# Kernel tuning notes

Measured on AMD Instinct MI355X. Metric: run time of the kernel, lower is better.

The kernel has to match this reference:

```python
import jax, jax.numpy as jnp
import numpy as np

N = 100000      # nodes
E = 300000      # directed edges (avg degree ~3, ogbn-arxiv-like sparsity)
F_IN = 128      # ogbn-arxiv node features
H = 256         # hidden
C = 40          # ogbn-arxiv classes
L = 6           # num_layers
BN_EPS = 1e-5


def setup_inputs() -> dict:
    key = jax.random.key(0)
    ks = jax.random.split(key, 12)
    x = jax.random.normal(ks[0], (N, F_IN), jnp.float32)
    edge_index = jax.random.randint(ks[1], (2, E), 0, N, dtype=jnp.int32)
    s_in = 1.0 / np.sqrt(F_IN)
    s_h = 1.0 / np.sqrt(H)
    return {
        "x": x,
        "edge_index": edge_index,
        "w_in": jax.random.normal(ks[2], (F_IN, H), jnp.float32) * s_in,
        "b_in": jnp.zeros((H,), jnp.float32),
        "conv_w": jax.random.normal(ks[3], (L, H, H), jnp.float32) * s_h,
        "conv_b": jnp.zeros((L, H), jnp.float32),
        "bn_gamma": jnp.ones((L, H), jnp.float32),
        "bn_beta": jnp.zeros((L, H), jnp.float32),
        "out_w": jax.random.normal(ks[4], (H, C), jnp.float32) * s_h,
        "out_b": jnp.zeros((C,), jnp.float32),
        "res_weights": jax.random.normal(ks[5], (L,), jnp.float32),
    }


def _gcn_norm(edge_index, n_nodes):
    # GCNConv default: add self-loops, symmetric normalization D^-1/2 (A+I) D^-1/2
    loops = jnp.arange(n_nodes, dtype=edge_index.dtype)
    src = jnp.concatenate([edge_index[0], loops])
    dst = jnp.concatenate([edge_index[1], loops])
    deg = jax.ops.segment_sum(jnp.ones_like(dst, jnp.float32), dst, num_segments=n_nodes)
    dinv = jax.lax.rsqrt(jnp.maximum(deg, 1.0))
    norm = dinv[src] * dinv[dst]  # [E+N]
    return src, dst, norm


def _batchnorm(h, gamma, beta):
    # BatchNorm1d in training mode: biased batch statistics over nodes
    m = jnp.mean(h, axis=0)
    v = jnp.mean(jnp.square(h - m), axis=0)
    return (h - m) * jax.lax.rsqrt(v + BN_EPS) * gamma + beta


def reference(x, edge_index, w_in, b_in, conv_w, conv_b, bn_gamma, bn_beta, out_w, out_b, res_weights):
    src, dst, norm = _gcn_norm(edge_index, N)
    h = x @ w_in + b_in            # input_fc: [N, H]
    x_input = h
    layer_out = []
    prev = None
    for i in range(L):
        hw = h @ conv_w[i]                                  # linear transform
        msg = hw[src] * norm[:, None]                       # gather + scale
        agg = jax.ops.segment_sum(msg, dst, num_segments=N) + conv_b[i]  # scatter-add
        a = jax.nn.relu(_batchnorm(agg, bn_gamma[i], bn_beta[i]))
        # dropout p=0.5 omitted (eval mode / deterministic reference)
        if i == 0:
            h = a + 0.2 * x_input
        else:
            h = a + 0.2 * x_input + 0.7 * prev
        layer_out.append(h)
        prev = h
    w = jax.nn.softmax(res_weights)                          # [L]
    mix = jnp.einsum('lnh,l->nh', jnp.stack(layer_out), w)   # weighted sum of layer outputs
    logits = mix @ out_w + out_b                             # [N, C]
    return jax.nn.log_softmax(logits, axis=1)
```

## Files before the change

kernel.cpp:

```cpp
#include <hip/hip_runtime.h>
#include <math.h>

#define Nn   100000
#define Ee   300000
#define FIN  128
#define Hdim 256
#define Ncls 40
#define Lnum 6
#define SCAN_B 98
#define KP   264
#define EMAX 1152

typedef __attribute__((ext_vector_type(8))) short bf16x8;
typedef __attribute__((ext_vector_type(4))) float f32x4;

__device__ __forceinline__ float bf2f(unsigned int u16) {
    unsigned int x = u16 << 16;
    return __builtin_bit_cast(float, x);
}
__device__ __forceinline__ unsigned short f2bf(float f) {
    unsigned int x = __builtin_bit_cast(unsigned int, f);
    x = (x + 0x7FFFu + ((x >> 16) & 1u)) >> 16;
    return (unsigned short)x;
}
__device__ __forceinline__ void unpack2(unsigned int u, float& lo, float& hi) {
    lo = __builtin_bit_cast(float, u << 16);
    hi = __builtin_bit_cast(float, u & 0xFFFF0000u);
}
__device__ __forceinline__ unsigned int pack2(float a, float b) {
    return (unsigned int)f2bf(a) | ((unsigned int)f2bf(b) << 16);
}
__device__ __forceinline__ void acc8(float* a, float w, uint4 v) {
    float f0, f1;
    unpack2(v.x, f0, f1); a[0] += w * f0; a[1] += w * f1;
    unpack2(v.y, f0, f1); a[2] += w * f0; a[3] += w * f1;
    unpack2(v.z, f0, f1); a[4] += w * f0; a[5] += w * f1;
    unpack2(v.w, f0, f1); a[6] += w * f0; a[7] += w * f1;
}

__global__ void count_edges(const int* __restrict__ ei, int* __restrict__ cnt) {
    int e = blockIdx.x * blockDim.x + threadIdx.x;
    if (e < Ee) atomicAdd(&cnt[ei[Ee + e]], 1);
}

__global__ void scan_block(const int* __restrict__ cnt, int* __restrict__ iscan,
                           int* __restrict__ btot) {
    __shared__ int buf[1024];
    int t = threadIdx.x;
    int g = blockIdx.x * 1024 + t;
    int v = (g < Nn) ? cnt[g] : 0;
    buf[t] = v; __syncthreads();
    for (int off = 1; off < 1024; off <<= 1) {
        int x = buf[t];
        int a = (t >= off) ? buf[t - off] : 0;
        __syncthreads();
        buf[t] = x + a;
        __syncthreads();
    }
    if (g < Nn) iscan[g] = buf[t];
    if (t == 1023) btot[blockIdx.x] = buf[1023];
}

__global__ void scan_tops(const int* __restrict__ btot, int* __restrict__ bpref) {
    __shared__ int b[128];
    int t = threadIdx.x;
    int v = (t < SCAN_B) ? btot[t] : 0;
    b[t] = v; __syncthreads();
    for (int off = 1; off < 128; off <<= 1) {
        int x = b[t];
        int a = (t >= off) ? b[t - off] : 0;
        __syncthreads();
        b[t] = x + a;
        __syncthreads();
    }
    if (t < SCAN_B) bpref[t] = b[t] - v;
}

__global__ void scan_final(const int* __restrict__ cnt, const int* __restrict__ iscan,
                           const int* __restrict__ bpref, int* __restrict__ offs,
                           float* __restrict__ dinvp) {
    int g = blockIdx.x * 1024 + threadIdx.x;
    if (g < Nn) {
        int c = cnt[g];
        offs[g] = bpref[blockIdx.x] + iscan[g] - c;
        dinvp[g] = rsqrtf((float)(c + 1));
    }
    if (g == 0) offs[Nn] = Ee;
}

__global__ void fill_csr(const int* __restrict__ ei, const int* __restrict__ offs,
                         int* __restrict__ cur, const float* __restrict__ dinvp,
                         int* __restrict__ esrc, float* __restrict__ ew) {
    int e = blockIdx.x * blockDim.x + threadIdx.x;
    if (e >= Ee) return;
    int s = ei[e], d = ei[Ee + e];
    int p = offs[d] + atomicAdd(&cur[d], 1);
    esrc[p] = s;
    ew[p] = dinvp[s];
}

__global__ void prep_weights(const float* __restrict__ conv_w, const float* __restrict__ w_in,
                             const float* __restrict__ out_w,
                             unsigned short* __restrict__ Whi,
                             unsigned short* __restrict__ Fhi,
                             unsigned short* __restrict__ Whd, unsigned short* __restrict__ Wld) {
    int b = blockIdx.x, t = threadIdx.x;
    if (b < 1536) {
        int id = b * 256 + t;
        int l = id >> 16, k = (id >> 8) & 255, n = id & 255;
        Whi[l * 65536 + n * 256 + k] = f2bf(conv_w[id]);
    } else if (b < 1664) {
        int id = (b - 1536) * 256 + t;
        int k = id >> 8, n = id & 255;
        Fhi[n * FIN + k] = f2bf(w_in[id]);
    } else {
        int id = (b - 1664) * 256 + t;
        int c = id >> 8, k = id & 255;
        float w = (c < Ncls) ? out_w[k * Ncls + c] : 0.f;
        unsigned short hi = f2bf(w);
        unsigned short lo = f2bf(w - bf2f(hi));
        Whd[c * 256 + k] = hi;
        Wld[c * 256 + k] = lo;
    }
}

__global__ void cvt_bf16(const float* __restrict__ src, unsigned short* __restrict__ dst, int n8) {
    int i = blockIdx.x * blockDim.x + threadIdx.x;
    if (i >= n8) return;
    float4 a = ((const float4*)src)[i * 2];
    float4 b = ((const float4*)src)[i * 2 + 1];
    uint4 o;
    o.x = pack2(a.x, a.y); o.y = pack2(a.z, a.w);
    o.z = pack2(b.x, b.y); o.w = pack2(b.z, b.w);
    ((uint4*)dst)[i] = o;
}

__global__ __launch_bounds__(512) void gemm_mfma(
    const unsigned short* __restrict__ A, unsigned short* __restrict__ C,
    const unsigned short* __restrict__ W,
    const float* __restrict__ bias, int K, int nrows)
{
    __shared__ __align__(16) unsigned short smem[18432];

    const int t    = threadIdx.x;
    const int lane = t & 63, wid = t >> 6;
    const int ln   = lane & 15, quad = lane >> 4;
    const int r64  = (wid >> 2) * 64, c64 = (wid & 3) * 64;
    const int r0   = blockIdx.x * 128;

    unsigned short* At = smem;
    unsigned short* Bt = smem + 5120;

    f32x4 acc[4][4];
#pragma unroll
    for (int i = 0; i < 4; ++i)
#pragma unroll
        for (int j = 0; j < 4; ++j) acc[i][j] = (f32x4){0.f, 0.f, 0.f, 0.f};

    const int arow = t >> 2, akq = t & 3;
    const bool arow_ok = (r0 + arow < nrows);
    const int nk = K >> 5;

    uint4 ga = make_uint4(0u, 0u, 0u, 0u);
    if (arow_ok) ga = *(const uint4*)&A[(size_t)(r0 + arow) * K + akq * 8];
    uint4 gb[2];
#pragma unroll
    for (int q = 0; q < 2; ++q) {
        int idx = t + 512 * q, row = idx >> 2, kq = idx & 3;
        gb[q] = *(const uint4*)&W[(size_t)row * K + kq * 8];
    }

    for (int kt = 0; kt < nk; ++kt) {
        __syncthreads();
        *(uint4*)&At[arow * 40 + akq * 8] = ga;
#pragma unroll
        for (int q = 0; q < 2; ++q) {
            int idx = t + 512 * q, row = idx >> 2, kq = idx & 3;
            *(uint4*)&Bt[row * 40 + kq * 8] = gb[q];
        }
        __syncthreads();
        if (kt + 1 < nk) {
            int k0 = (kt + 1) << 5;
            ga = make_uint4(0u, 0u, 0u, 0u);
            if (arow_ok) ga = *(const uint4*)&A[(size_t)(r0 + arow) * K + k0 + akq * 8];
#pragma unroll
            for (int q = 0; q < 2; ++q) {
                int idx = t + 512 * q, row = idx >> 2, kq = idx & 3;
                gb[q] = *(const uint4*)&W[(size_t)row * K + k0 + kq * 8];
            }
        }
        bf16x8 af[4], bf[4];
#pragma unroll
        for (int rt = 0; rt < 4; ++rt)
            af[rt] = *(const bf16x8*)&At[(r64 + rt * 16 + ln) * 40 + quad * 8];
#pragma unroll
        for (int ct = 0; ct < 4; ++ct)
            bf[ct] = *(const bf16x8*)&Bt[(c64 + ct * 16 + ln) * 40 + quad * 8];
#pragma unroll
        for (int rt = 0; rt < 4; ++rt)
#pragma unroll
            for (int ct = 0; ct < 4; ++ct)
                acc[rt][ct] = __builtin_amdgcn_mfma_f32_16x16x32_bf16(af[rt], bf[ct], acc[rt][ct], 0, 0, 0);
    }
    __syncthreads();

    float bc[4];
#pragma unroll
    for (int ct = 0; ct < 4; ++ct) bc[ct] = bias[c64 + ct * 16 + ln];

    unsigned short* Tt = &smem[wid * 2304];
    const int rr2 = lane & 31, jh = lane >> 5;
#pragma unroll
    for (int h = 0; h < 2; ++h) {
#pragma unroll
        for (int rr = 0; rr < 2; ++rr) {
            int rt = 2 * h + rr;
#pragma unroll
            for (int ct = 0; ct < 4; ++ct)
#pragma unroll
                for (int v = 0; v < 4; ++v)
                    Tt[(rr * 16 + quad * 4 + v) * 72 + ct * 16 + ln] = f2bf(acc[rt][ct][v] + bc[ct]);
        }
        __asm__ volatile("s_waitcnt lgkmcnt(0)" ::: "memory");
        int grow = r0 + r64 + h * 32 + rr2;
        if (grow < nrows) {
#pragma unroll
            for (int j = 0; j < 4; ++j) {
                uint4 v4 = *(const uint4*)&Tt[rr2 * 72 + jh * 32 + j * 8];
                *(uint4*)&C[(size_t)grow * 256 + c64 + jh * 32 + j * 8] = v4;
            }
        }
        __asm__ volatile("s_waitcnt lgkmcnt(0)" ::: "memory");
    }
}

__global__ __launch_bounds__(512, 4) void gemm_agg(
    const unsigned short* __restrict__ Hin,
    unsigned short* __restrict__ C,
    const unsigned short* __restrict__ W,
    const float* __restrict__ bias,
    const int* __restrict__ offs, const int* __restrict__ esrc,
    const float* __restrict__ ew, const float* __restrict__ dinvp,
    float* __restrict__ bnsum, float* __restrict__ bnsq)
{
    __shared__ __align__(16) unsigned short At[128 * KP];
    __shared__ __align__(16) uint2 eL[EMAX];
    __shared__ int oL[132];
    __shared__ float lsum[256], lsq[256];

    const int t    = threadIdx.x;
    const int lane = t & 63, wid = t >> 6;
    const int ln   = lane & 15, quad = lane >> 4;
    const int r64  = (wid >> 2) * 64, c64 = (wid & 3) * 64;
    const int r0   = blockIdx.x * 128;

    if (t < 256) { lsum[t] = 0.f; lsq[t] = 0.f; }

    const int rEnd = (r0 + 128 <= Nn) ? (r0 + 128) : Nn;
    const int E0 = offs[r0];
    const int E1 = offs[rEnd];
    const int nE = E1 - E0;
    const bool staged = (nE <= EMAX);

    if (t < 129) {
        int idx = r0 + t; if (idx > Nn) idx = Nn;
        oL[t] = offs[idx];
    }
    if (staged) {
        for (int j = t; j < nE; j += 512)
            eL[j] = make_uint2((unsigned)esrc[E0 + j],
                               __builtin_bit_cast(unsigned, ew[E0 + j]));
    }
    __syncthreads();

    const int half = lane >> 5, l31 = lane & 31;
#pragma unroll 1
    for (int pr = 0; pr < 8; ++pr) {
        int lrow = wid * 16 + pr * 2 + half;
        int n = r0 + lrow;
        float a[8] = {0.f, 0.f, 0.f, 0.f, 0.f, 0.f, 0.f, 0.f};
        if (n < Nn) {
            int o0 = oL[lrow], o1 = oL[lrow + 1];
            float dn = dinvp[n];
            uint4 u = *(const uint4*)&Hin[(size_t)n * Hdim + l31 * 8];
            acc8(a, dn, u);
            if (staged) {
                int e = o0;
                if (e < o1) {
                    uint2 sw = eL[e - E0];
                    uint4 v  = *(const uint4*)&Hin[(size_t)sw.x * Hdim + l31 * 8];
                    float w  = __builtin_bit_cast(float, sw.y);
                    for (++e; e < o1; ++e) {
                        uint2 sw2 = eL[e - E0];
                        uint4 v2  = *(const uint4*)&Hin[(size_t)sw2.x * Hdim + l31 * 8];
                        acc8(a, w, v);
                        v = v2; w = __builtin_bit_cast(float, sw2.y);
                    }
                    acc8(a, w, v);
                }
            } else {
                for (int e = o0; e < o1; ++e) {
                    int s = esrc[e];
                    float w = ew[e];
                    uint4 v = *(const uint4*)&Hin[(size_t)s * Hdim + l31 * 8];
                    acc8(a, w, v);
                }
            }
#pragma unroll
            for (int k = 0; k < 8; ++k) a[k] *= dn;
        }
        *(uint4*)&At[lrow * KP + l31 * 8] =
            make_uint4(pack2(a[0], a[1]), pack2(a[2], a[3]),
                       pack2(a[4], a[5]), pack2(a[6], a[7]));
    }
    __syncthreads();

    f32x4 acc[4][4];
#pragma unroll
    for (int i = 0; i < 4; ++i)
#pragma unroll
        for (int j = 0; j < 4; ++j) acc[i][j] = (f32x4){0.f, 0.f, 0.f, 0.f};

#pragma unroll
    for (int kt = 0; kt < 8; ++kt) {
        bf16x8 af[4], bf[4];
#pragma unroll
        for (int ct = 0; ct < 4; ++ct)
            bf[ct] = *(const bf16x8*)&W[(size_t)(c64 + ct * 16 + ln) * 256 + kt * 32 + quad * 8];
#pragma unroll
        for (int rt = 0; rt < 4; ++rt)
            af[rt] = *(const bf16x8*)&At[(r64 + rt * 16 + ln) * KP + kt * 32 + quad * 8];
#pragma unroll
        for (int rt = 0; rt < 4; ++rt)
#pragma unroll
            for (int ct = 0; ct < 4; ++ct)
                acc[rt][ct] = __builtin_amdgcn_mfma_f32_16x16x32_bf16(af[rt], bf[ct], acc[rt][ct], 0, 0, 0);
    }

    float bc[4];
#pragma unroll
    for (int ct = 0; ct < 4; ++ct) bc[ct] = bias[c64 + ct * 16 + ln];

#pragma unroll
    for (int ct = 0; ct < 4; ++ct) {
        float s = 0.f, qq = 0.f;
#pragma unroll
        for (int rt = 0; rt < 4; ++rt)
#pragma unroll
            for (int v = 0; v < 4; ++v) {
                int row = r0 + r64 + rt * 16 + quad * 4 + v;
                if (row < Nn) {
                    float val = acc[rt][ct][v] + bc[ct];
                    s += val; qq += val * val;
                }
            }
        s  += __shfl_xor(s, 16);  s  += __shfl_xor(s, 32);
        qq += __shfl_xor(qq, 16); qq += __shfl_xor(qq, 32);
        if (quad == 0) { atomicAdd(&lsum[c64 + ct * 16 + ln], s); atomicAdd(&lsq[c64 + ct * 16 + ln], qq); }
    }

    __syncthreads();

#pragma unroll
    for (int rt = 0; rt < 4; ++rt)
#pragma unroll
        for (int ct = 0; ct < 4; ++ct)
#pragma unroll
            for (int v = 0; v < 4; ++v)
                At[(r64 + rt * 16 + quad * 4 + v) * KP + c64 + ct * 16 + ln] =
                    f2bf(acc[rt][ct][v] + bc[ct]);
    __syncthreads();

    const int l31s = t & 31, rhalf = t >> 5;
#pragma unroll
    for (int p = 0; p < 8; ++p) {
        int lrow = p * 16 + rhalf;
        int grow = r0 + lrow;
        if (grow < Nn) {
            uint4 v4 = *(const uint4*)&At[lrow * KP + l31s * 8];
            *(uint4*)&C[(size_t)grow * 256 + l31s * 8] = v4;
        }
    }

    if (t < 256) {
        atomicAdd(&bnsum[t], lsum[t]);
        atomicAdd(&bnsq[t], lsq[t]);
    }
}

__global__ void apply_kernel(const unsigned short* __restrict__ T,
                             const unsigned short* __restrict__ X,
                             unsigned short* __restrict__ Hb, unsigned short* __restrict__ M,
                             const float* __restrict__ bnsum, const float* __restrict__ bnsq,
                             const float* __restrict__ gamma, const float* __restrict__ beta,
                             const float* __restrict__ res_w, int layer) {
    __shared__ float sc[256], sh[256];
    int t = threadIdx.x;
    {
        float mean = bnsum[t] * (1.0f / Nn);
        float var  = fmaxf(bnsq[t] * (1.0f / Nn) - mean * mean, 0.f);
        float rstd = rsqrtf(var + 1e-5f);
        float s = gamma[t] * rstd;
        sc[t] = s; sh[t] = beta[t] - mean * s;
    }
    float m0 = res_w[0];
#pragma unroll
    for (int i = 1; i < Lnum; ++i) m0 = fmaxf(m0, res_w[i]);
    float se = 0.f, wl = 0.f;
#pragma unroll
    for (int i = 0; i < Lnum; ++i) {
        float e = __expf(res_w[i] - m0);
        se += e;
        if (i == layer) wl = e;
    }
    float wi = wl / se;
    __syncthreads();

    int idx = blockIdx.x * blockDim.x + t;
    int c8 = idx & 31;
    float scl[8], shl[8];
#pragma unroll
    for (int k = 0; k < 8; ++k) { scl[k] = sc[c8 * 8 + k]; shl[k] = sh[c8 * 8 + k]; }

    uint4 tv = ((const uint4*)T)[idx];
    uint4 xv = ((const uint4*)X)[idx];
    float tf[8], xf[8];
    unpack2(tv.x, tf[0], tf[1]); unpack2(tv.y, tf[2], tf[3]);
    unpack2(tv.z, tf[4], tf[5]); unpack2(tv.w, tf[6], tf[7]);
    unpack2(xv.x, xf[0], xf[1]); unpack2(xv.y, xf[2], xf[3]);
    unpack2(xv.z, xf[4], xf[5]); unpack2(xv.w, xf[6], xf[7]);

    float a[8];
#pragma unroll
    for (int k = 0; k < 8; ++k)
        a[k] = fmaxf(tf[k] * scl[k] + shl[k], 0.f) + 0.2f * xf[k];
    if (layer > 0) {
        uint4 hv = ((const uint4*)Hb)[idx];
        float hf[8];
        unpack2(hv.x, hf[0], hf[1]); unpack2(hv.y, hf[2], hf[3]);
        unpack2(hv.z, hf[4], hf[5]); unpack2(hv.w, hf[6], hf[7]);
#pragma unroll
        for (int k = 0; k < 8; ++k) a[k] += 0.7f * hf[k];
    }
    uint4 ho;
    ho.x = pack2(a[0], a[1]); ho.y = pack2(a[2], a[3]);
    ho.z = pack2(a[4], a[5]); ho.w = pack2(a[6], a[7]);
    ((uint4*)Hb)[idx] = ho;

    float m[8];
    if (layer == 0) {
#pragma unroll
        for (int k = 0; k < 8; ++k) m[k] = wi * a[k];
    } else {
        uint4 mv = ((const uint4*)M)[idx];
        float mf[8];
        unpack2(mv.x, mf[0], mf[1]); unpack2(mv.y, mf[2], mf[3]);
        unpack2(mv.z, mf[4], mf[5]); unpack2(mv.w, mf[6], mf[7]);
#pragma unroll
        for (int k = 0; k < 8; ++k) m[k] = mf[k] + wi * a[k];
    }
    uint4 mo;
    mo.x = pack2(m[0], m[1]); mo.y = pack2(m[2], m[3]);
    mo.z = pack2(m[4], m[5]); mo.w = pack2(m[6], m[7]);
    ((uint4*)M)[idx] = mo;
}

__global__ __launch_bounds__(512) void head_mfma(const unsigned short* __restrict__ M,
                                                 const unsigned short* __restrict__ Whd,
                                                 const unsigned short* __restrict__ Wld,
                                                 const float* __restrict__ out_b,
                                                 float* __restrict__ out, int nrows) {
    __shared__ unsigned short At[128 * 40];
    const int t    = threadIdx.x;
    const int lane = t & 63, wid = t >> 6;
    const int ln   = lane & 15, quad = lane >> 4;
    const int r0   = blockIdx.x * 128;

    f32x4 acc[3];
#pragma unroll
    for (int ct = 0; ct < 3; ++ct) acc[ct] = (f32x4){0.f, 0.f, 0.f, 0.f};

    for (int k0 = 0; k0 < 256; k0 += 32) {
        __syncthreads();
        {
            int row = t >> 2, kq = t & 3;
            uint4 g = make_uint4(0u, 0u, 0u, 0u);
            if (r0 + row < nrows)
                g = *(const uint4*)&M[(size_t)(r0 + row) * 256 + k0 + kq * 8];
            *(uint4*)&At[row * 40 + kq * 8] = g;
        }
        __syncthreads();
        bf16x8 af = *(const bf16x8*)&At[(wid * 16 + ln) * 40 + quad * 8];
#pragma unroll
        for (int ct = 0; ct < 3; ++ct) {
            int c = ct * 16 + ln;
            bf16x8 bh = *(const bf16x8*)&Whd[c * 256 + k0 + quad * 8];
            bf16x8 bl = *(const bf16x8*)&Wld[c * 256 + k0 + quad * 8];
            acc[ct] = __builtin_amdgcn_mfma_f32_16x16x32_bf16(af, bh, acc[ct], 0, 0, 0);
            acc[ct] = __builtin_amdgcn_mfma_f32_16x16x32_bf16(af, bl, acc[ct], 0, 0, 0);
        }
    }

    int   cc[3]; float bias[3];
#pragma unroll
    for (int ct = 0; ct < 3; ++ct) {
        cc[ct] = ct * 16 + ln;
        bias[ct] = (cc[ct] < Ncls) ? out_b[cc[ct]] : 0.f;
    }
#pragma unroll
    for (int v = 0; v < 4; ++v) {
        int row = r0 + wid * 16 + quad * 4 + v;
        float val[3];
#pragma unroll
        for (int ct = 0; ct < 3; ++ct) val[ct] = acc[ct][v] + bias[ct];
        float mx = -1e30f;
#pragma unroll
        for (int ct = 0; ct < 3; ++ct) if (cc[ct] < Ncls) mx = fmaxf(mx, val[ct]);
        mx = fmaxf(mx, __shfl_xor(mx, 1)); mx = fmaxf(mx, __shfl_xor(mx, 2));
        mx = fmaxf(mx, __shfl_xor(mx, 4)); mx = fmaxf(mx, __shfl_xor(mx, 8));
        float s = 0.f;
#pragma unroll
        for (int ct = 0; ct < 3; ++ct) if (cc[ct] < Ncls) s += __expf(val[ct] - mx);
        s += __shfl_xor(s, 1); s += __shfl_xor(s, 2);
        s += __shfl_xor(s, 4); s += __shfl_xor(s, 8);
        float lse = mx + __logf(s);
        if (row < nrows) {
            out[(size_t)row * Ncls + cc[0]] = val[0] - lse;
            out[(size_t)row * Ncls + cc[1]] = val[1] - lse;
            if (ln < 8) out[(size_t)row * Ncls + cc[2]] = val[2] - lse;
        }
    }
}

extern "C" void kernel_launch(void* const* d_in, const int* in_sizes, int n_in,
                              void* d_out, int out_size, void* d_ws, size_t ws_size,
                              hipStream_t stream)
{
    const float* x      = (const float*)d_in[0];
    const int*   ei     = (const int*)d_in[1];
    const float* w_in   = (const float*)d_in[2];
    const float* b_in   = (const float*)d_in[3];
    const float* conv_w = (const float*)d_in[4];
    const float* conv_b = (const float*)d_in[5];
    const float* gamma  = (const float*)d_in[6];
    const float* beta   = (const float*)d_in[7];
    const float* out_w  = (const float*)d_in[8];
    const float* out_b  = (const float*)d_in[9];
    const float* res_w  = (const float*)d_in[10];
    float* out = (float*)d_out;
    char* ws = (char*)d_ws;

    int*   cnt    = (int*)  (ws + 0);
    int*   cursor = (int*)  (ws + 400000);
    int*   offs   = (int*)  (ws + 800000);
    float* dinvp  = (float*)(ws + 1200016);
    int*   esrc   = (int*)  (ws + 1600016);
    float* ew     = (float*)(ws + 2800016);
    int*   iscan  = (int*)  (ws + 4002064);
    int*   btot   = (int*)  (ws + 4402064);
    int*   bpref  = (int*)  (ws + 4402576);
    unsigned short* Whi = (unsigned short*)(ws + 4403088);
    unsigned short* Fhi = (unsigned short*)(ws + 5975952);
    unsigned short* Whd = (unsigned short*)(ws + 6107024);
    unsigned short* Wld = (unsigned short*)(ws + 6131600);
    unsigned short* X   = (unsigned short*)(ws + 6156176);
    unsigned short* Hb  = X  + (size_t)Nn * Hdim;
    unsigned short* T   = Hb + (size_t)Nn * Hdim;
    unsigned short* M   = T  + (size_t)Nn * Hdim;
    unsigned short* xbf = M;

    float* bnA = (float*)(ws + 4002064);

    const int gblocks = (Nn + 127) / 128;

    hipMemsetAsync(cnt, 0, 800000, stream);

    count_edges<<<(Ee + 255) / 256, 256, 0, stream>>>(ei, cnt);
    scan_block<<<SCAN_B, 1024, 0, stream>>>(cnt, iscan, btot);
    scan_tops<<<1, 128, 0, stream>>>(btot, bpref);
    scan_final<<<SCAN_B, 1024, 0, stream>>>(cnt, iscan, bpref, offs, dinvp);
    fill_csr<<<(Ee + 255) / 256, 256, 0, stream>>>(ei, offs, cursor, dinvp, esrc, ew);

    hipMemsetAsync(bnA, 0, Lnum * 512 * sizeof(float), stream);

    prep_weights<<<1712, 256, 0, stream>>>(conv_w, w_in, out_w,
                                           Whi, Fhi, Whd, Wld);
    cvt_bf16<<<(Nn * FIN / 8 + 255) / 256, 256, 0, stream>>>(x, xbf, Nn * FIN / 8);

    gemm_mfma<<<gblocks, 512, 0, stream>>>(xbf, X, Fhi, b_in, FIN, Nn);

    for (int i = 0; i < Lnum; ++i) {
        float* bnsumL = bnA + (size_t)i * 512;
        float* bnsqL  = bnsumL + 256;
        gemm_agg<<<gblocks, 512, 0, stream>>>(i == 0 ? X : Hb, T,
                                              Whi + (size_t)i * Hdim * Hdim,
                                              conv_b + (size_t)i * Hdim,
                                              offs, esrc, ew, dinvp,
                                              bnsumL, bnsqL);
        apply_kernel<<<(Nn * 32) / 256, 256, 0, stream>>>(T, X, Hb, M,
                                                          bnsumL, bnsqL,
                                                          gamma + (size_t)i * Hdim,
                                                          beta + (size_t)i * Hdim,
                                                          res_w, i);
    }

    head_mfma<<<gblocks, 512, 0, stream>>>(M, Whd, Wld, out_b, out, Nn);
}
```

Baseline: 1.094 ms.

## Interleave two-row gather in aggregation and replace BN atomics with partial-sum reduction

The aggregation phase of gemm_agg now processes two destination rows per half-wave in an interleaved loop, so two independent neighbor gathers are in flight at once to hide memory latency. Batch-norm statistics are written per block into a partial buffer and summed by a new bn_reduce kernel instead of 782 blocks doing global atomics on the same 512 addresses. This adds an extra kernel launch per layer and depends on the workspace being large enough, falling back to atomics otherwise. Divergence grows when the two rows have different degrees.

Measured after the change: 1.033 ms. -5.5%, faster.

```diff
diff --git a/kernel.cpp b/kernel.cpp
--- a/kernel.cpp
+++ b/kernel.cpp
@@ -135,6 +135,23 @@
     ((uint4*)dst)[i] = o;
 }
 
+__global__ void bn_reduce(const float* __restrict__ P, float* __restrict__ bnsum,
+                          float* __restrict__ bnsq, int nb) {
+    int c = threadIdx.x;
+    int per = (nb + gridDim.x - 1) / gridDim.x;
+    int r0 = blockIdx.x * per;
+    int r1 = r0 + per; if (r1 > nb) r1 = nb;
+    float s = 0.f, q = 0.f;
+    for (int r = r0; r < r1; ++r) {
+        s += P[(size_t)r * 512 + c];
+        q += P[(size_t)r * 512 + 256 + c];
+    }
+    if (r0 < r1) {
+        atomicAdd(&bnsum[c], s);
+        atomicAdd(&bnsq[c], q);
+    }
+}
+
 __global__ __launch_bounds__(512) void gemm_mfma(
     const unsigned short* __restrict__ A, unsigned short* __restrict__ C,
     const unsigned short* __restrict__ W,
@@ -241,7 +258,8 @@
     const float* __restrict__ bias,
     const int* __restrict__ offs, const int* __restrict__ esrc,
     const float* __restrict__ ew, const float* __restrict__ dinvp,
-    float* __restrict__ bnsum, float* __restrict__ bnsq)
+    float* __restrict__ bnsum, float* __restrict__ bnsq,
+    float* __restrict__ Pstats)
 {
     __shared__ __align__(16) unsigned short At[128 * KP];
     __shared__ __align__(16) uint2 eL[EMAX];
@@ -274,44 +292,63 @@
     __syncthreads();
 
     const int half = lane >> 5, l31 = lane & 31;
+    const int base = wid * 16 + half * 8;
 #pragma unroll 1
-    for (int pr = 0; pr < 8; ++pr) {
-        int lrow = wid * 16 + pr * 2 + half;
-        int n = r0 + lrow;
-        float a[8] = {0.f, 0.f, 0.f, 0.f, 0.f, 0.f, 0.f, 0.f};
-        if (n < Nn) {
-            int o0 = oL[lrow], o1 = oL[lrow + 1];
-            float dn = dinvp[n];
-            uint4 u = *(const uint4*)&Hin[(size_t)n * Hdim + l31 * 8];
-            acc8(a, dn, u);
-            if (staged) {
-                int e = o0;
-                if (e < o1) {
-                    uint2 sw = eL[e - E0];
-                    uint4 v  = *(const uint4*)&Hin[(size_t)sw.x * Hdim + l31 * 8];
-                    float w  = __builtin_bit_cast(float, sw.y);
-                    for (++e; e < o1; ++e) {
-                        uint2 sw2 = eL[e - E0];
-                        uint4 v2  = *(const uint4*)&Hin[(size_t)sw2.x * Hdim + l31 * 8];
-                        acc8(a, w, v);
-                        v = v2; w = __builtin_bit_cast(float, sw2.y);
-                    }
-                    acc8(a, w, v);
+    for (int p = 0; p < 4; ++p) {
+        const int rA = base + 2 * p, rB = rA + 1;
+        const int nA = r0 + rA, nB = r0 + rB;
+        float a[8] = {0.f,0.f,0.f,0.f,0.f,0.f,0.f,0.f};
+        float b[8] = {0.f,0.f,0.f,0.f,0.f,0.f,0.f,0.f};
+        int eA = oL[rA], eA1 = oL[rA + 1];
+        int eB = oL[rB], eB1 = oL[rB + 1];
+        float dnA = 0.f, dnB = 0.f;
+        if (nA < Nn) {
+            dnA = dinvp[nA];
+            uint4 u = *(const uint4*)&Hin[(size_t)nA * Hdim + l31 * 8];
+            acc8(a, dnA, u);
+        }
+        if (nB < Nn) {
+            dnB = dinvp[nB];
+            uint4 u = *(const uint4*)&Hin[(size_t)nB * Hdim + l31 * 8];
+            acc8(b, dnB, u);
+        }
+        if (staged) {
+            while (eA < eA1 || eB < eB1) {
+                bool dA = eA < eA1, dB = eB < eB1;
+                uint4 vA, vB; float wA = 0.f, wB = 0.f;
+                if (dA) {
+                    uint2 s = eL[eA - E0];
+                    wA = __builtin_bit_cast(float, s.y);
+                    vA = *(const uint4*)&Hin[(size_t)s.x * Hdim + l31 * 8];
                 }
-            } else {
-                for (int e = o0; e < o1; ++e) {
-                    int s = esrc[e];
-                    float w = ew[e];
-                    uint4 v = *(const uint4*)&Hin[(size_t)s * Hdim + l31 * 8];
-                    acc8(a, w, v);
+                if (dB) {
+                    uint2 s = eL[eB - E0];
+                    wB = __builtin_bit_cast(float, s.y);
+                    vB = *(const uint4*)&Hin[(size_t)s.x * Hdim + l31 * 8];
                 }
+                if (dA) { acc8(a, wA, vA); ++eA; }
+                if (dB) { acc8(b, wB, vB); ++eB; }
             }
-#pragma unroll
-            for (int k = 0; k < 8; ++k) a[k] *= dn;
-        }
-        *(uint4*)&At[lrow * KP + l31 * 8] =
+        } else {
+            for (int e = eA; e < eA1; ++e) {
+                int s = esrc[e]; float w = ew[e];
+                uint4 v = *(const uint4*)&Hin[(size_t)s * Hdim + l31 * 8];
+                acc8(a, w, v);
+            }
+            for (int e = eB; e < eB1; ++e) {
+                int s = esrc[e]; float w = ew[e];
+                uint4 v = *(const uint4*)&Hin[(size_t)s * Hdim + l31 * 8];
+                acc8(b, w, v);
+            }
+        }
+#pragma unroll
+        for (int k = 0; k < 8; ++k) { a[k] *= dnA; b[k] *= dnB; }
+        *(uint4*)&At[rA * KP + l31 * 8] =
             make_uint4(pack2(a[0], a[1]), pack2(a[2], a[3]),
                        pack2(a[4], a[5]), pack2(a[6], a[7]));
+        *(uint4*)&At[rB * KP + l31 * 8] =
+            make_uint4(pack2(b[0], b[1]), pack2(b[2], b[3]),
+                       pack2(b[4], b[5]), pack2(b[6], b[7]));
     }
     __syncthreads();
 
@@ -383,8 +420,13 @@
     }
 
     if (t < 256) {
-        atomicAdd(&bnsum[t], lsum[t]);
-        atomicAdd(&bnsq[t], lsq[t]);
+        if (Pstats) {
+            Pstats[(size_t)blockIdx.x * 512 + t]       = lsum[t];
+            Pstats[(size_t)blockIdx.x * 512 + 256 + t] = lsq[t];
+        } else {
+            atomicAdd(&bnsum[t], lsum[t]);
+            atomicAdd(&bnsq[t], lsq[t]);
+        }
     }
 }
 
@@ -573,6 +615,10 @@
 
     const int gblocks = (Nn + 127) / 128;
 
+    const size_t P_OFS = 6156176 + 4 * (size_t)Nn * Hdim * sizeof(unsigned short);
+    const size_t P_BYTES = (size_t)gblocks * 512 * sizeof(float);
+    float* Pst = (ws_size >= P_OFS + P_BYTES) ? (float*)(ws + P_OFS) : nullptr;
+
     hipMemsetAsync(cnt, 0, 800000, stream);
 
     count_edges<<<(Ee + 255) / 256, 256, 0, stream>>>(ei, cnt);
@@ -596,7 +642,9 @@
                                               Whi + (size_t)i * Hdim * Hdim,
                                               conv_b + (size_t)i * Hdim,
                                               offs, esrc, ew, dinvp,
-                                              bnsumL, bnsqL);
+                                              bnsumL, bnsqL, Pst);
+        if (Pst)
+            bn_reduce<<<64, 256, 0, stream>>>(Pst, bnsumL, bnsqL, gblocks);
         apply_kernel<<<(Nn * 32) / 256, 256, 0, stream>>>(T, X, Hb, M,
                                                           bnsumL, bnsqL,
                                                           gamma + (size_t)i * Hdim,
```
